# Kernel optimization log

Measured on AMD Instinct MI355X. Metric: run time of the kernel, lower is better.

## Reference

```python
import jax, jax.numpy as jnp
import numpy as np

# Dims: batch B, query len SQ, key len SK, hidden D, heads H, head dim DH
B, SQ, SK, D, H = 8, 1024, 1024, 1024, 8
DH = D // H
KERN_EPS = 1e-6
LN_EPS = 1e-5


def _layer_norm(x, gamma, beta):
    m = x.mean(-1, keepdims=True)
    v = ((x - m) ** 2).mean(-1, keepdims=True)
    return (x - m) * jax.lax.rsqrt(v + LN_EPS) * gamma + beta


def setup_inputs() -> dict:
    key = jax.random.key(0)
    ks = jax.random.split(key, 16)
    s = 0.02  # param init scale
    return {
        "key_in": jax.random.normal(ks[0], (B, SK, 1), jnp.float32),
        "query_in": jax.random.normal(ks[1], (B, SQ, 1), jnp.float32),
        "value_in": jax.random.normal(ks[2], (B, SK, D), jnp.float32),
        "residual": jax.random.normal(ks[3], (B, SQ, D), jnp.float32),
        # projections (bias=False for key/value/query, matching torch Linear)
        "Wk": jax.random.normal(ks[4], (1, H), jnp.float32) * s,
        "Wq": jax.random.normal(ks[5], (1, H), jnp.float32) * s,
        "Wv": jax.random.normal(ks[6], (D, D), jnp.float32) * s,
        "Wf": jax.random.normal(ks[7], (D, D), jnp.float32) * s,
        "bf": jnp.zeros((D,), jnp.float32),
        "g1": jnp.ones((D,), jnp.float32),
        "b1": jnp.zeros((D,), jnp.float32),
        # MLP with 2 hidden layers (ReLU) + output layer
        "Wm1": jax.random.normal(ks[8], (D, D), jnp.float32) * s,
        "bm1": jnp.zeros((D,), jnp.float32),
        "Wm2": jax.random.normal(ks[9], (D, D), jnp.float32) * s,
        "bm2": jnp.zeros((D,), jnp.float32),
        "Wm3": jax.random.normal(ks[10], (D, D), jnp.float32) * s,
        "bm3": jnp.zeros((D,), jnp.float32),
        "g2": jnp.ones((D,), jnp.float32),
        "b2": jnp.zeros((D,), jnp.float32),
    }


def reference(key_in, query_in, value_in, residual, Wk, Wq, Wv, Wf, bf,
              g1, b1, Wm1, bm1, Wm2, bm2, Wm3, bm3, g2, b2):
    k = key_in @ Wk      # [B, SK, H] per-head scalar key coordinates
    q = query_in @ Wq    # [B, SQ, H]
    v = value_in @ Wv    # [B, SK, D]
    # Normalized Fourier kernel attention: cos kernel between per-head
    # scalar query/key coordinates, normalized over keys.
    kern = jnp.cos(q[:, :, None, :] - k[:, None, :, :])             # [B,SQ,SK,H]
    att = kern / (jnp.abs(kern).sum(axis=2, keepdims=True) + KERN_EPS)
    vh = v.reshape(B, SK, H, DH)
    out = jnp.einsum('bqkh,bkhd->bqhd', att, vh).reshape(B, SQ, D)
    out = out @ Wf + bf
    x = _layer_norm(residual + out, g1, b1)
    h1 = jax.nn.relu(x @ Wm1 + bm1)
    h2 = jax.nn.relu(h1 @ Wm2 + bm2)
    mlp_out = h2 @ Wm3 + bm3
    return _layer_norm(x + mlp_out, g2, b2)
```

## Files before the change

kernel.cpp:

```cpp
#include <hip/hip_runtime.h>
#include <math.h>

#define B_ 8
#define SQn 1024
#define SKn 1024
#define Dn 1024
#define Hn 8
#define DHn 128

#define OFF_CQ 0
#define OFF_SQ 65536
#define OFF_CK 131072
#define OFF_SK 196608
#define OFF_PC 262144
#define OFF_PS 327680
#define OFF_CV 393216
#define OFF_SV 401408
#define OFF_M  409600
#define OFF_DEN 540672
#define OFF_X  606208
#define OFF_H1 8994816
#define OFF_WT 17383424

typedef __attribute__((ext_vector_type(8))) short short8;
typedef __attribute__((ext_vector_type(4))) float f32x4;

__device__ __forceinline__ unsigned short f2bf(float f) {
    unsigned int u = __float_as_uint(f);
    unsigned int r = (u + 0x7fffu + ((u >> 16) & 1u)) >> 16;
    return (unsigned short)r;
}
__device__ __forceinline__ float bf2f(unsigned short h) {
    return __uint_as_float(((unsigned int)h) << 16);
}

__device__ __forceinline__ void gld16(const unsigned short* g, unsigned short* l) {
    __builtin_amdgcn_global_load_lds(
        (const __attribute__((address_space(1))) void*)g,
        (__attribute__((address_space(3))) void*)l, 16, 0, 0);
}

__global__ void k_prep(const float* __restrict__ key_in, const float* __restrict__ query_in,
                       const float* __restrict__ Wk, const float* __restrict__ Wq,
                       const float* __restrict__ W0, const float* __restrict__ W1,
                       const float* __restrict__ W2, float* __restrict__ ws,
                       unsigned short* __restrict__ wt) {
    __shared__ float tile[64][65];
    const int bid = blockIdx.x;
    const int tid = threadIdx.x;
    if (bid < 512) {
        int idx = bid * 256 + tid;
        const int n = B_ * SQn * Hn;
        if (idx < n) {
            int h = idx & 7, bs = idx >> 3;
            float v = query_in[bs] * Wq[h];
            ws[OFF_CQ + idx] = cosf(v);
            ws[OFF_SQ + idx] = sinf(v);
        } else {
            int i2 = idx - n;
            int h = i2 & 7, bs = i2 >> 3;
            float v = key_in[bs] * Wk[h];
            ws[OFF_CK + i2] = cosf(v);
            ws[OFF_SK + i2] = sinf(v);
        }
    } else if (bid < 1280) {
        const int zb = bid - 512;
        const int z = zb >> 8, r = zb & 255;
        const float* W = (z == 0) ? W0 : (z == 1) ? W1 : W2;
        unsigned short* out = wt + (size_t)z * 2097152;
        const int k0 = (r & 15) * 64, n0 = (r >> 4) * 64;
        const int tx = tid & 63, ty = tid >> 6;
        #pragma unroll
        for (int i = 0; i < 16; ++i) {
            int rr = ty + i * 4;
            tile[rr][tx] = W[(size_t)(k0 + rr) * Dn + n0 + tx];
        }
        __syncthreads();
        #pragma unroll
        for (int i = 0; i < 16; ++i) {
            int rr = ty + i * 4;
            float v = tile[tx][rr];
            unsigned short hi = f2bf(v);
            unsigned short lo = f2bf(v - bf2f(hi));
            out[(size_t)(n0 + rr) * 2048 + k0 + tx] = hi;
            out[(size_t)(n0 + rr) * 2048 + 1024 + k0 + tx] = lo;
        }
    } else {
        const int zb = bid - 1280;
        float4* p = (float4*)(ws + OFF_PC);
        p[zb * 256 + tid] = (float4){0.f, 0.f, 0.f, 0.f};
    }
}

__global__ void k_phase(const float* __restrict__ value_in, const float* __restrict__ ck,
                        const float* __restrict__ sk, float* __restrict__ Pc,
                        float* __restrict__ Ps) {
    __shared__ __align__(16) float ckk[512];
    __shared__ __align__(16) float skk[512];
    const int b = blockIdx.x, it = blockIdx.y, kc = blockIdx.z;
    const int tid = threadIdx.x;
    const int base = (b * SKn + kc * 64) * Hn;
    *(float2*)&ckk[tid * 2] = *(const float2*)&ck[base + tid * 2];
    *(float2*)&skk[tid * 2] = *(const float2*)&sk[base + tid * 2];
    __syncthreads();
    const int i = it * 256 + tid;
    float aC[8] = {0,0,0,0,0,0,0,0}, aS[8] = {0,0,0,0,0,0,0,0};
    const float* vp = value_in + (size_t)(b * SKn + kc * 64) * Dn + i;
    #pragma unroll 4
    for (int kk = 0; kk < 64; ++kk) {
        float v = vp[(size_t)kk * Dn];
        float4 c0 = *(const float4*)&ckk[kk * 8];
        float4 c1 = *(const float4*)&ckk[kk * 8 + 4];
        float4 s0 = *(const float4*)&skk[kk * 8];
        float4 s1 = *(const float4*)&skk[kk * 8 + 4];
        aC[0] = fmaf(v, c0.x, aC[0]); aC[1] = fmaf(v, c0.y, aC[1]);
        aC[2] = fmaf(v, c0.z, aC[2]); aC[3] = fmaf(v, c0.w, aC[3]);
        aC[4] = fmaf(v, c1.x, aC[4]); aC[5] = fmaf(v, c1.y, aC[5]);
        aC[6] = fmaf(v, c1.z, aC[6]); aC[7] = fmaf(v, c1.w, aC[7]);
        aS[0] = fmaf(v, s0.x, aS[0]); aS[1] = fmaf(v, s0.y, aS[1]);
        aS[2] = fmaf(v, s0.z, aS[2]); aS[3] = fmaf(v, s0.w, aS[3]);
        aS[4] = fmaf(v, s1.x, aS[4]); aS[5] = fmaf(v, s1.y, aS[5]);
        aS[6] = fmaf(v, s1.z, aS[6]); aS[7] = fmaf(v, s1.w, aS[7]);
    }
    #pragma unroll
    for (int h = 0; h < 8; ++h) {
        atomicAdd(&Pc[(b * Hn + h) * Dn + i], aC[h]);
        atomicAdd(&Ps[(b * Hn + h) * Dn + i], aS[h]);
    }
}

__global__ void k_cv(const float* __restrict__ Pc, const float* __restrict__ Ps,
                     const float* __restrict__ Wv, float* __restrict__ Cv,
                     float* __restrict__ Sv) {
    const int bh = blockIdx.x;
    const int ic = blockIdx.y;
    const int h = bh & 7;
    const int d = threadIdx.x;
    float ac = 0.f, as = 0.f;
    const float* wp = Wv + (size_t)(ic * 64) * Dn + h * DHn + d;
    const float* pc = Pc + bh * Dn + ic * 64;
    const float* ps = Ps + bh * Dn + ic * 64;
    #pragma unroll 4
    for (int i = 0; i < 64; ++i) {
        float w = wp[(size_t)i * Dn];
        ac = fmaf(pc[i], w, ac);
        as = fmaf(ps[i], w, as);
    }
    atomicAdd(&Cv[bh * DHn + d], ac);
    atomicAdd(&Sv[bh * DHn + d], as);
}

__global__ void k_m(const float* __restrict__ Cv, const float* __restrict__ Sv,
                    const float* __restrict__ Wf, float* __restrict__ M) {
    const int bh = blockIdx.x;
    const int dc = blockIdx.y;
    const int b = bh >> 3, h = bh & 7;
    const int j = threadIdx.x * 4;
    float4 ac = {0,0,0,0}, as = {0,0,0,0};
    #pragma unroll 4
    for (int dd = 0; dd < 32; ++dd) {
        int d = dc * 32 + dd;
        float cv = Cv[bh * DHn + d];
        float sv = Sv[bh * DHn + d];
        float4 w = *(const float4*)&Wf[(size_t)(h * DHn + d) * Dn + j];
        ac.x = fmaf(cv, w.x, ac.x); ac.y = fmaf(cv, w.y, ac.y);
        ac.z = fmaf(cv, w.z, ac.z); ac.w = fmaf(cv, w.w, ac.w);
        as.x = fmaf(sv, w.x, as.x); as.y = fmaf(sv, w.y, as.y);
        as.z = fmaf(sv, w.z, as.z); as.w = fmaf(sv, w.w, as.w);
    }
    float* mc = &M[(size_t)(b * 16 + h) * Dn + j];
    float* ms = &M[(size_t)(b * 16 + 8 + h) * Dn + j];
    atomicAdd(mc + 0, ac.x); atomicAdd(mc + 1, ac.y);
    atomicAdd(mc + 2, ac.z); atomicAdd(mc + 3, ac.w);
    atomicAdd(ms + 0, as.x); atomicAdd(ms + 1, as.y);
    atomicAdd(ms + 2, as.z); atomicAdd(ms + 3, as.w);
}

__global__ void k_denom(const float* __restrict__ ws, float* __restrict__ den) {
    __shared__ __align__(16) float ckk[8][132];
    __shared__ __align__(16) float skk[8][132];
    const int b = blockIdx.x, qt = blockIdx.y, zh = blockIdx.z;
    const int tid = threadIdx.x;
    const int qq = tid >> 3, h = tid & 7;
    const int q = qt * 32 + qq;
    const float cqv = ws[OFF_CQ + (b * SQn + q) * Hn + h];
    const float sqv = ws[OFF_SQ + (b * SQn + q) * Hn + h];
    float acc = 0.f;
    for (int kc = zh * 4; kc < zh * 4 + 4; ++kc) {
        __syncthreads();
        const int base = (b * SKn + kc * 128) * Hn;
        float4 c4 = *(const float4*)&ws[OFF_CK + base + tid * 4];
        float4 s4 = *(const float4*)&ws[OFF_SK + base + tid * 4];
        #pragma unroll
        for (int u = 0; u < 4; ++u) {
            int f = tid * 4 + u;
            ckk[f & 7][f >> 3] = ((const float*)&c4)[u];
            skk[f & 7][f >> 3] = ((const float*)&s4)[u];
        }
        __syncthreads();
        #pragma unroll
        for (int kv = 0; kv < 32; ++kv) {
            float4 c = *(const float4*)&ckk[h][kv * 4];
            float4 s = *(const float4*)&skk[h][kv * 4];
            acc += fabsf(cqv * c.x + sqv * s.x);
            acc += fabsf(cqv * c.y + sqv * s.y);
            acc += fabsf(cqv * c.z + sqv * s.z);
            acc += fabsf(cqv * c.w + sqv * s.w);
        }
    }
    atomicAdd(&den[(b * SQn + q) * Hn + h], acc);
}

__device__ inline void block_ln_stats(float lsum, float lsq, float* red,
                                      float& mean, float& rstd) {
    #pragma unroll
    for (int off = 32; off; off >>= 1) {
        lsum += __shfl_xor(lsum, off);
        lsq  += __shfl_xor(lsq, off);
    }
    const int wid = threadIdx.x >> 6;
    if ((threadIdx.x & 63) == 0) { red[wid * 2] = lsum; red[wid * 2 + 1] = lsq; }
    __syncthreads();
    if (threadIdx.x == 0) {
        float s  = red[0] + red[2] + red[4] + red[6];
        float ss = red[1] + red[3] + red[5] + red[7];
        float m = s * (1.0f / Dn);
        red[8] = m;
        red[9] = rsqrtf(ss * (1.0f / Dn) - m * m + 1e-5f);
    }
    __syncthreads();
    mean = red[8];
    rstd = red[9];
}

__global__ void k_x(const float* __restrict__ residual, const float* __restrict__ bf,
                    const float* __restrict__ g1, const float* __restrict__ b1,
                    const float* __restrict__ ws, unsigned short* __restrict__ Xp) {
    __shared__ float lcoef[16];
    __shared__ float red[12];
    const int bq = blockIdx.x;
    const int b = bq >> 10;
    const int tid = threadIdx.x;
    if (tid < 8) {
        float dinv = 1.0f / (ws[OFF_DEN + bq * Hn + tid] + 1e-6f);
        lcoef[tid]     = ws[OFF_CQ + bq * Hn + tid] * dinv;
        lcoef[8 + tid] = ws[OFF_SQ + bq * Hn + tid] * dinv;
    }
    __syncthreads();
    const int j = tid * 4;
    float4 acc = *(const float4*)&bf[j];
    const float* Mp = ws + OFF_M + (size_t)b * 16 * Dn + j;
    #pragma unroll
    for (int t = 0; t < 16; ++t) {
        float cf = lcoef[t];
        float4 m4 = *(const float4*)&Mp[(size_t)t * Dn];
        acc.x = fmaf(cf, m4.x, acc.x); acc.y = fmaf(cf, m4.y, acc.y);
        acc.z = fmaf(cf, m4.z, acc.z); acc.w = fmaf(cf, m4.w, acc.w);
    }
    float4 r = *(const float4*)&residual[(size_t)bq * Dn + j];
    acc.x += r.x; acc.y += r.y; acc.z += r.z; acc.w += r.w;
    float lsum = acc.x + acc.y + acc.z + acc.w;
    float lsq = acc.x * acc.x + acc.y * acc.y + acc.z * acc.z + acc.w * acc.w;
    float mean, rstd;
    block_ln_stats(lsum, lsq, red, mean, rstd);
    float4 g = *(const float4*)&g1[j];
    float4 be = *(const float4*)&b1[j];
    float o[4];
    o[0] = (acc.x - mean) * rstd * g.x + be.x;
    o[1] = (acc.y - mean) * rstd * g.y + be.y;
    o[2] = (acc.z - mean) * rstd * g.z + be.z;
    o[3] = (acc.w - mean) * rstd * g.w + be.w;
    ushort4 hi, lo;
    unsigned short* hp = (unsigned short*)&hi;
    unsigned short* lp = (unsigned short*)&lo;
    #pragma unroll
    for (int u = 0; u < 4; ++u) {
        hp[u] = f2bf(o[u]);
        lp[u] = f2bf(o[u] - bf2f(hp[u]));
    }
    *(ushort4*)&Xp[(size_t)bq * 2048 + j] = hi;
    *(ushort4*)&Xp[(size_t)bq * 2048 + 1024 + j] = lo;
}

__global__ __launch_bounds__(256) void gemm_split(const unsigned short* __restrict__ Ap,
                                                  const unsigned short* __restrict__ Wp,
                                                  const float* __restrict__ bias,
                                                  unsigned short* __restrict__ Cp,
                                                  unsigned short* __restrict__ Cb, int mode) {
    __shared__ __align__(16) unsigned short buf[2][4][128 * 32];
    const int t = threadIdx.x;
    const int orig = blockIdx.x;
    const int c = orig & 7, g = orig >> 3;
    const int m0 = (c * 8 + (g & 7)) * 128;
    const int n0 = (g >> 3) * 128;

    const int w = t >> 6;
    const int wm = (w >> 1) * 64;
    const int wn = (w & 1) * 64;
    const int l15 = t & 15;
    const int kq = (t >> 4) & 3;

    const int tr2 = t >> 2;
    const int tc2 = (t & 3) * 8;

    f32x4 acc[4][4];
    #pragma unroll
    for (int m = 0; m < 4; ++m)
        #pragma unroll
        for (int n = 0; n < 4; ++n)
            acc[m][n] = (f32x4){0.f, 0.f, 0.f, 0.f};

#define STAGE(pp, kh) do {                                                          \
        const int k0_ = (kh) * 32;                                                  \
        _Pragma("unroll")                                                           \
        for (int i_ = 0; i_ < 2; ++i_) {                                            \
            const int row_ = i_ * 64 + tr2;                                         \
            gld16(Ap + (size_t)(m0 + row_) * 2048 + k0_ + tc2,                      \
                  &buf[pp][0][row_ * 32 + tc2]);                                    \
            gld16(Ap + (size_t)(m0 + row_) * 2048 + 1024 + k0_ + tc2,               \
                  &buf[pp][1][row_ * 32 + tc2]);                                    \
            gld16(Wp + (size_t)(n0 + row_) * 2048 + k0_ + tc2,                      \
                  &buf[pp][2][row_ * 32 + tc2]);                                    \
            gld16(Wp + (size_t)(n0 + row_) * 2048 + 1024 + k0_ + tc2,               \
                  &buf[pp][3][row_ * 32 + tc2]);                                    \
        }                                                                           \
    } while (0)

    STAGE(0, 0);
    __syncthreads();
    for (int kh = 0; kh < 32; ++kh) {
        const int cur = kh & 1;
        if (kh < 31) STAGE(cur ^ 1, kh + 1);
        short8 afh[4], afl[4], bfh[4], bfl[4];
        #pragma unroll
        for (int m = 0; m < 4; ++m) {
            const int ro = (wm + m * 16 + l15) * 32 + kq * 8;
            afh[m] = *(const short8*)&buf[cur][0][ro];
            afl[m] = *(const short8*)&buf[cur][1][ro];
        }
        #pragma unroll
        for (int n = 0; n < 4; ++n) {
            const int ro = (wn + n * 16 + l15) * 32 + kq * 8;
            bfh[n] = *(const short8*)&buf[cur][2][ro];
            bfl[n] = *(const short8*)&buf[cur][3][ro];
        }
        #pragma unroll
        for (int m = 0; m < 4; ++m)
            #pragma unroll
            for (int n = 0; n < 4; ++n) {
                acc[m][n] = __builtin_amdgcn_mfma_f32_16x16x32_bf16(
                    afh[m], bfh[n], acc[m][n], 0, 0, 0);
                acc[m][n] = __builtin_amdgcn_mfma_f32_16x16x32_bf16(
                    afl[m], bfh[n], acc[m][n], 0, 0, 0);
                acc[m][n] = __builtin_amdgcn_mfma_f32_16x16x32_bf16(
                    afh[m], bfl[n], acc[m][n], 0, 0, 0);
            }
        __syncthreads();
    }
#undef STAGE

    #pragma unroll
    for (int n = 0; n < 4; ++n) {
        const int col = n0 + wn + n * 16 + l15;
        const float bv = bias[col];
        #pragma unroll
        for (int m = 0; m < 4; ++m) {
            #pragma unroll
            for (int r = 0; r < 4; ++r) {
                const int row = m0 + wm + m * 16 + kq * 4 + r;
                float cc = acc[m][n][r] + bv;
                if (mode == 0) {
                    cc = fmaxf(cc, 0.f);
                    unsigned short hi = f2bf(cc);
                    unsigned short lo = f2bf(cc - bf2f(hi));
                    Cp[(size_t)row * 2048 + col] = hi;
                    Cp[(size_t)row * 2048 + 1024 + col] = lo;
                } else {
                    Cb[(size_t)row * 1024 + col] = f2bf(cc);
                }
            }
        }
    }
}

__global__ void k_final(const unsigned short* __restrict__ Xp,
                        const unsigned short* __restrict__ Y,
                        const float* __restrict__ g2, const float* __restrict__ b2,
                        float* __restrict__ out) {
    __shared__ float red[12];
    const int bq = blockIdx.x;
    const int tid = threadIdx.x;
    const int j = tid * 4;
    ushort4 xh = *(const ushort4*)&Xp[(size_t)bq * 2048 + j];
    ushort4 xl = *(const ushort4*)&Xp[(size_t)bq * 2048 + 1024 + j];
    ushort4 yv = *(const ushort4*)&Y[(size_t)bq * 1024 + j];
    float xv[4];
    xv[0] = bf2f(xh.x) + bf2f(xl.x) + bf2f(yv.x);
    xv[1] = bf2f(xh.y) + bf2f(xl.y) + bf2f(yv.y);
    xv[2] = bf2f(xh.z) + bf2f(xl.z) + bf2f(yv.z);
    xv[3] = bf2f(xh.w) + bf2f(xl.w) + bf2f(yv.w);
    float lsum = xv[0] + xv[1] + xv[2] + xv[3];
    float lsq = xv[0]*xv[0] + xv[1]*xv[1] + xv[2]*xv[2] + xv[3]*xv[3];
    float mean, rstd;
    block_ln_stats(lsum, lsq, red, mean, rstd);
    float4 g = *(const float4*)&g2[j];
    float4 be = *(const float4*)&b2[j];
    float4 o;
    o.x = (xv[0] - mean) * rstd * g.x + be.x;
    o.y = (xv[1] - mean) * rstd * g.y + be.y;
    o.z = (xv[2] - mean) * rstd * g.z + be.z;
    o.w = (xv[3] - mean) * rstd * g.w + be.w;
    *(float4*)&out[(size_t)bq * Dn + j] = o;
}

extern "C" void kernel_launch(void* const* d_in, const int* in_sizes, int n_in,
                              void* d_out, int out_size, void* d_ws, size_t ws_size,
                              hipStream_t stream) {
    const float* key_in   = (const float*)d_in[0];
    const float* query_in = (const float*)d_in[1];
    const float* value_in = (const float*)d_in[2];
    const float* residual = (const float*)d_in[3];
    const float* Wk  = (const float*)d_in[4];
    const float* Wq  = (const float*)d_in[5];
    const float* Wv  = (const float*)d_in[6];
    const float* Wf  = (const float*)d_in[7];
    const float* bf  = (const float*)d_in[8];
    const float* g1  = (const float*)d_in[9];
    const float* b1  = (const float*)d_in[10];
    const float* Wm1 = (const float*)d_in[11];
    const float* bm1 = (const float*)d_in[12];
    const float* Wm2 = (const float*)d_in[13];
    const float* bm2 = (const float*)d_in[14];
    const float* Wm3 = (const float*)d_in[15];
    const float* bm3 = (const float*)d_in[16];
    const float* g2  = (const float*)d_in[17];
    const float* b2  = (const float*)d_in[18];
    float* ws  = (float*)d_ws;
    float* out = (float*)d_out;

    unsigned short* Xp  = (unsigned short*)(ws + OFF_X);
    unsigned short* H1p = (unsigned short*)(ws + OFF_H1);
    unsigned short* H2p = (unsigned short*)out;
    unsigned short* Yb  = (unsigned short*)(ws + OFF_H1);
    unsigned short* WT  = (unsigned short*)(ws + OFF_WT);

    k_prep<<<1364, 256, 0, stream>>>(key_in, query_in, Wk, Wq, Wm1, Wm2, Wm3, ws, WT);
    k_phase<<<dim3(8, 4, 16), 256, 0, stream>>>(value_in, ws + OFF_CK, ws + OFF_SK,
                                                ws + OFF_PC, ws + OFF_PS);
    k_cv<<<dim3(64, 16), 128, 0, stream>>>(ws + OFF_PC, ws + OFF_PS, Wv,
                                           ws + OFF_CV, ws + OFF_SV);
    k_m<<<dim3(64, 4), 256, 0, stream>>>(ws + OFF_CV, ws + OFF_SV, Wf, ws + OFF_M);
    k_denom<<<dim3(8, 32, 2), 256, 0, stream>>>(ws, ws + OFF_DEN);
    k_x<<<8192, 256, 0, stream>>>(residual, bf, g1, b1, ws, Xp);

    gemm_split<<<512, 256, 0, stream>>>(Xp, WT, bm1, H1p, nullptr, 0);
    gemm_split<<<512, 256, 0, stream>>>(H1p, WT + 2097152, bm2, H2p, nullptr, 0);
    gemm_split<<<512, 256, 0, stream>>>(H2p, WT + 2 * 2097152, bm3, nullptr, Yb, 1);
    k_final<<<8192, 256, 0, stream>>>(Xp, Yb, g2, b2, out);
}
```

Baseline: 401.3 us.

## Merge phase and denominator kernels, replace atomics with partials, loosen GEMM barriers

Fuses the k_phase and k_denom launches into one kernel, k_pd, that picks its work by block index. This removes one launch and lets both independent workloads run at the same time. The phase part now writes per-key-chunk partial sums to scratch instead of using atomicAdd, and k_cv reduces those 16 partials before the Wv contraction. In the split GEMM main loop, __syncthreads is replaced by explicit vmcnt waits plus s_barrier/sched_barrier, so the next tile's loads can stay in flight during the MFMAs. The zeroing region and the k_prep grid change to match the new buffer layout.

```diff
diff --git a/kernel.cpp b/kernel.cpp
--- a/kernel.cpp
+++ b/kernel.cpp
@@ -12,8 +12,6 @@
 #define OFF_SQ 65536
 #define OFF_CK 131072
 #define OFF_SK 196608
-#define OFF_PC 262144
-#define OFF_PS 327680
 #define OFF_CV 393216
 #define OFF_SV 401408
 #define OFF_M  409600
@@ -87,64 +85,115 @@
         }
     } else {
         const int zb = bid - 1280;
-        float4* p = (float4*)(ws + OFF_PC);
+        float4* p = (float4*)(ws + OFF_CV);
         p[zb * 256 + tid] = (float4){0.f, 0.f, 0.f, 0.f};
     }
 }
 
-__global__ void k_phase(const float* __restrict__ value_in, const float* __restrict__ ck,
-                        const float* __restrict__ sk, float* __restrict__ Pc,
-                        float* __restrict__ Ps) {
-    __shared__ __align__(16) float ckk[512];
-    __shared__ __align__(16) float skk[512];
-    const int b = blockIdx.x, it = blockIdx.y, kc = blockIdx.z;
+__global__ void k_pd(const float* __restrict__ value_in, const float* __restrict__ ws,
+                     float* __restrict__ Pcp, float* __restrict__ Psp,
+                     float* __restrict__ den) {
+    __shared__ __align__(16) float sA[8][132];
+    __shared__ __align__(16) float sB[8][132];
+    const int bid = blockIdx.x;
     const int tid = threadIdx.x;
-    const int base = (b * SKn + kc * 64) * Hn;
-    *(float2*)&ckk[tid * 2] = *(const float2*)&ck[base + tid * 2];
-    *(float2*)&skk[tid * 2] = *(const float2*)&sk[base + tid * 2];
-    __syncthreads();
-    const int i = it * 256 + tid;
-    float aC[8] = {0,0,0,0,0,0,0,0}, aS[8] = {0,0,0,0,0,0,0,0};
-    const float* vp = value_in + (size_t)(b * SKn + kc * 64) * Dn + i;
-    #pragma unroll 4
-    for (int kk = 0; kk < 64; ++kk) {
-        float v = vp[(size_t)kk * Dn];
-        float4 c0 = *(const float4*)&ckk[kk * 8];
-        float4 c1 = *(const float4*)&ckk[kk * 8 + 4];
-        float4 s0 = *(const float4*)&skk[kk * 8];
-        float4 s1 = *(const float4*)&skk[kk * 8 + 4];
-        aC[0] = fmaf(v, c0.x, aC[0]); aC[1] = fmaf(v, c0.y, aC[1]);
-        aC[2] = fmaf(v, c0.z, aC[2]); aC[3] = fmaf(v, c0.w, aC[3]);
-        aC[4] = fmaf(v, c1.x, aC[4]); aC[5] = fmaf(v, c1.y, aC[5]);
-        aC[6] = fmaf(v, c1.z, aC[6]); aC[7] = fmaf(v, c1.w, aC[7]);
-        aS[0] = fmaf(v, s0.x, aS[0]); aS[1] = fmaf(v, s0.y, aS[1]);
-        aS[2] = fmaf(v, s0.z, aS[2]); aS[3] = fmaf(v, s0.w, aS[3]);
-        aS[4] = fmaf(v, s1.x, aS[4]); aS[5] = fmaf(v, s1.y, aS[5]);
-        aS[6] = fmaf(v, s1.z, aS[6]); aS[7] = fmaf(v, s1.w, aS[7]);
-    }
-    #pragma unroll
-    for (int h = 0; h < 8; ++h) {
-        atomicAdd(&Pc[(b * Hn + h) * Dn + i], aC[h]);
-        atomicAdd(&Ps[(b * Hn + h) * Dn + i], aS[h]);
-    }
-}
-
-__global__ void k_cv(const float* __restrict__ Pc, const float* __restrict__ Ps,
+    if (bid < 512) {
+        const int b = bid & 7, it = (bid >> 3) & 3, kc = bid >> 5;
+        float* ckk = (float*)sA;
+        float* skk = (float*)sB;
+        const float* ck = ws + OFF_CK;
+        const float* sk = ws + OFF_SK;
+        const int base = (b * SKn + kc * 64) * Hn;
+        *(float2*)&ckk[tid * 2] = *(const float2*)&ck[base + tid * 2];
+        *(float2*)&skk[tid * 2] = *(const float2*)&sk[base + tid * 2];
+        __syncthreads();
+        const int i = it * 256 + tid;
+        float aC[8] = {0,0,0,0,0,0,0,0}, aS[8] = {0,0,0,0,0,0,0,0};
+        const float* vp = value_in + (size_t)(b * SKn + kc * 64) * Dn + i;
+        #pragma unroll 4
+        for (int kk = 0; kk < 64; ++kk) {
+            float v = vp[(size_t)kk * Dn];
+            float4 c0 = *(const float4*)&ckk[kk * 8];
+            float4 c1 = *(const float4*)&ckk[kk * 8 + 4];
+            float4 s0 = *(const float4*)&skk[kk * 8];
+            float4 s1 = *(const float4*)&skk[kk * 8 + 4];
+            aC[0] = fmaf(v, c0.x, aC[0]); aC[1] = fmaf(v, c0.y, aC[1]);
+            aC[2] = fmaf(v, c0.z, aC[2]); aC[3] = fmaf(v, c0.w, aC[3]);
+            aC[4] = fmaf(v, c1.x, aC[4]); aC[5] = fmaf(v, c1.y, aC[5]);
+            aC[6] = fmaf(v, c1.z, aC[6]); aC[7] = fmaf(v, c1.w, aC[7]);
+            aS[0] = fmaf(v, s0.x, aS[0]); aS[1] = fmaf(v, s0.y, aS[1]);
+            aS[2] = fmaf(v, s0.z, aS[2]); aS[3] = fmaf(v, s0.w, aS[3]);
+            aS[4] = fmaf(v, s1.x, aS[4]); aS[5] = fmaf(v, s1.y, aS[5]);
+            aS[6] = fmaf(v, s1.z, aS[6]); aS[7] = fmaf(v, s1.w, aS[7]);
+        }
+        #pragma unroll
+        for (int h = 0; h < 8; ++h) {
+            Pcp[(size_t)(kc * 64 + b * 8 + h) * 1024 + i] = aC[h];
+            Psp[(size_t)(kc * 64 + b * 8 + h) * 1024 + i] = aS[h];
+        }
+    } else {
+        const int v = bid - 512;
+        const int b = v & 7, qt = (v >> 3) & 31, zh = v >> 8;
+        const int qq = tid >> 3, h = tid & 7;
+        const int q = qt * 32 + qq;
+        const float cqv = ws[OFF_CQ + (b * SQn + q) * Hn + h];
+        const float sqv = ws[OFF_SQ + (b * SQn + q) * Hn + h];
+        float acc = 0.f;
+        for (int kc = zh * 4; kc < zh * 4 + 4; ++kc) {
+            __syncthreads();
+            const int base = (b * SKn + kc * 128) * Hn;
+            float4 c4 = *(const float4*)&ws[OFF_CK + base + tid * 4];
+            float4 s4 = *(const float4*)&ws[OFF_SK + base + tid * 4];
+            #pragma unroll
+            for (int u = 0; u < 4; ++u) {
+                int f = tid * 4 + u;
+                sA[f & 7][f >> 3] = ((const float*)&c4)[u];
+                sB[f & 7][f >> 3] = ((const float*)&s4)[u];
+            }
+            __syncthreads();
+            #pragma unroll
+            for (int kv = 0; kv < 32; ++kv) {
+                float4 c = *(const float4*)&sA[h][kv * 4];
+                float4 s = *(const float4*)&sB[h][kv * 4];
+                acc += fabsf(cqv * c.x + sqv * s.x);
+                acc += fabsf(cqv * c.y + sqv * s.y);
+                acc += fabsf(cqv * c.z + sqv * s.z);
+                acc += fabsf(cqv * c.w + sqv * s.w);
+            }
+        }
+        atomicAdd(&den[(b * SQn + q) * Hn + h], acc);
+    }
+}
+
+__global__ void k_cv(const float* __restrict__ Pcp, const float* __restrict__ Psp,
                      const float* __restrict__ Wv, float* __restrict__ Cv,
                      float* __restrict__ Sv) {
+    __shared__ float pc2[2][64];
+    __shared__ float ps2[2][64];
     const int bh = blockIdx.x;
     const int ic = blockIdx.y;
     const int h = bh & 7;
-    const int d = threadIdx.x;
+    const int t = threadIdx.x;
+    {
+        const int ii = t & 63, kh2 = t >> 6;
+        float sc = 0.f, ss = 0.f;
+        #pragma unroll
+        for (int kc = kh2 * 8; kc < kh2 * 8 + 8; ++kc) {
+            sc += Pcp[(size_t)(kc * 64 + bh) * 1024 + ic * 64 + ii];
+            ss += Psp[(size_t)(kc * 64 + bh) * 1024 + ic * 64 + ii];
+        }
+        pc2[kh2][ii] = sc;
+        ps2[kh2][ii] = ss;
+    }
+    __syncthreads();
+    const int d = t;
     float ac = 0.f, as = 0.f;
     const float* wp = Wv + (size_t)(ic * 64) * Dn + h * DHn + d;
-    const float* pc = Pc + bh * Dn + ic * 64;
-    const float* ps = Ps + bh * Dn + ic * 64;
     #pragma unroll 4
     for (int i = 0; i < 64; ++i) {
         float w = wp[(size_t)i * Dn];
-        ac = fmaf(pc[i], w, ac);
-        as = fmaf(ps[i], w, as);
+        ac = fmaf(pc2[0][i] + pc2[1][i], w, ac);
+        as = fmaf(ps2[0][i] + ps2[1][i], w, as);
     }
     atomicAdd(&Cv[bh * DHn + d], ac);
     atomicAdd(&Sv[bh * DHn + d], as);
@@ -174,41 +223,6 @@
     atomicAdd(mc + 2, ac.z); atomicAdd(mc + 3, ac.w);
     atomicAdd(ms + 0, as.x); atomicAdd(ms + 1, as.y);
     atomicAdd(ms + 2, as.z); atomicAdd(ms + 3, as.w);
-}
-
-__global__ void k_denom(const float* __restrict__ ws, float* __restrict__ den) {
-    __shared__ __align__(16) float ckk[8][132];
-    __shared__ __align__(16) float skk[8][132];
-    const int b = blockIdx.x, qt = blockIdx.y, zh = blockIdx.z;
-    const int tid = threadIdx.x;
-    const int qq = tid >> 3, h = tid & 7;
-    const int q = qt * 32 + qq;
-    const float cqv = ws[OFF_CQ + (b * SQn + q) * Hn + h];
-    const float sqv = ws[OFF_SQ + (b * SQn + q) * Hn + h];
-    float acc = 0.f;
-    for (int kc = zh * 4; kc < zh * 4 + 4; ++kc) {
-        __syncthreads();
-        const int base = (b * SKn + kc * 128) * Hn;
-        float4 c4 = *(const float4*)&ws[OFF_CK + base + tid * 4];
-        float4 s4 = *(const float4*)&ws[OFF_SK + base + tid * 4];
-        #pragma unroll
-        for (int u = 0; u < 4; ++u) {
-            int f = tid * 4 + u;
-            ckk[f & 7][f >> 3] = ((const float*)&c4)[u];
-            skk[f & 7][f >> 3] = ((const float*)&s4)[u];
-        }
-        __syncthreads();
-        #pragma unroll
-        for (int kv = 0; kv < 32; ++kv) {
-            float4 c = *(const float4*)&ckk[h][kv * 4];
-            float4 s = *(const float4*)&skk[h][kv * 4];
-            acc += fabsf(cqv * c.x + sqv * s.x);
-            acc += fabsf(cqv * c.y + sqv * s.y);
-            acc += fabsf(cqv * c.z + sqv * s.z);
-            acc += fabsf(cqv * c.w + sqv * s.w);
-        }
-    }
-    atomicAdd(&den[(b * SQn + q) * Hn + h], acc);
 }
 
 __device__ inline void block_ln_stats(float lsum, float lsq, float* red,
@@ -327,10 +341,16 @@
     } while (0)
 
     STAGE(0, 0);
-    __syncthreads();
     for (int kh = 0; kh < 32; ++kh) {
         const int cur = kh & 1;
-        if (kh < 31) STAGE(cur ^ 1, kh + 1);
+        if (kh < 31) {
+            STAGE(cur ^ 1, kh + 1);
+            asm volatile("s_waitcnt vmcnt(8)" ::: "memory");
+        } else {
+            asm volatile("s_waitcnt vmcnt(0)" ::: "memory");
+        }
+        __builtin_amdgcn_s_barrier();
+        __builtin_amdgcn_sched_barrier(0);
         short8 afh[4], afl[4], bfh[4], bfl[4];
         #pragma unroll
         for (int m = 0; m < 4; ++m) {
@@ -355,7 +375,8 @@
                 acc[m][n] = __builtin_amdgcn_mfma_f32_16x16x32_bf16(
                     afh[m], bfl[n], acc[m][n], 0, 0, 0);
             }
-        __syncthreads();
+        __builtin_amdgcn_sched_barrier(0);
+        __builtin_amdgcn_s_barrier();
     }
 #undef STAGE
 
@@ -443,14 +464,13 @@
     unsigned short* H2p = (unsigned short*)out;
     unsigned short* Yb  = (unsigned short*)(ws + OFF_H1);
     unsigned short* WT  = (unsigned short*)(ws + OFF_WT);
-
-    k_prep<<<1364, 256, 0, stream>>>(key_in, query_in, Wk, Wq, Wm1, Wm2, Wm3, ws, WT);
-    k_phase<<<dim3(8, 4, 16), 256, 0, stream>>>(value_in, ws + OFF_CK, ws + OFF_SK,
-                                                ws + OFF_PC, ws + OFF_PS);
-    k_cv<<<dim3(64, 16), 128, 0, stream>>>(ws + OFF_PC, ws + OFF_PS, Wv,
-                                           ws + OFF_CV, ws + OFF_SV);
+    float* Pcp = ws + OFF_X;
+    float* Psp = ws + OFF_X + 1048576;
+
+    k_prep<<<1488, 256, 0, stream>>>(key_in, query_in, Wk, Wq, Wm1, Wm2, Wm3, ws, WT);
+    k_pd<<<1024, 256, 0, stream>>>(value_in, ws, Pcp, Psp, ws + OFF_DEN);
+    k_cv<<<dim3(64, 16), 128, 0, stream>>>(Pcp, Psp, Wv, ws + OFF_CV, ws + OFF_SV);
     k_m<<<dim3(64, 4), 256, 0, stream>>>(ws + OFF_CV, ws + OFF_SV, Wf, ws + OFF_M);
-    k_denom<<<dim3(8, 32, 2), 256, 0, stream>>>(ws, ws + OFF_DEN);
     k_x<<<8192, 256, 0, stream>>>(residual, bf, g1, b1, ws, Xp);
 
     gemm_split<<<512, 256, 0, stream>>>(Xp, WT, bm1, H1p, nullptr, 0);
```

Result: no change. 395.0 us (-1.6%).
